# Kernel optimization log

Hardware: AMD Instinct MI355X
Metric: run time of the kernel (lower is better)

The kernel has to match this reference:

```python
import jax, jax.numpy as jnp
import numpy as np

# Forest layout: 6 levels, children of node i at level L are contiguous at level L+1.
LEVEL_SIZES = [4096, 16384, 65536, 131072, 262144, 262144]
OFF = np.concatenate([[0], np.cumsum(LEVEL_SIZES)]).astype(np.int64)
N_NODES = int(OFF[-1])
VOCAB = 50000
D_IN = 128
HID = 128
N_CLASS = 4
W_SCALE = 0.08  # keep gate pre-activations in a sane range


def setup_inputs() -> dict:
    key = jax.random.key(0)
    ks = jax.random.split(key, 24)
    inp = {}
    inp["sen"] = jax.random.randint(ks[0], (N_NODES,), 0, VOCAB, dtype=jnp.int32)
    inp["embedding"] = jax.random.normal(ks[1], (VOCAB, D_IN), jnp.float32)
    names = ["ix", "ih", "fx", "fh", "ox", "oh", "ux", "uh"]
    for j, nm in enumerate(names):
        din = D_IN if nm.endswith("x") else HID
        inp["W_" + nm] = jax.random.normal(ks[2 + j], (din, HID), jnp.float32) * W_SCALE
        inp["b_" + nm] = jnp.zeros((HID,), jnp.float32)
    inp["W_out"] = jax.random.normal(ks[20], (HID, N_CLASS), jnp.float32) * W_SCALE
    inp["b_out"] = jnp.zeros((N_CLASS,), jnp.float32)
    return inp


def _forward(sen, embedding, W_ix, b_ix, W_ih, b_ih, W_fx, b_fx, W_fh, b_fh,
             W_ox, b_ox, W_oh, b_oh, W_ux, b_ux, W_uh, b_uh, W_out, b_out):
    emb = embedding[sen]                               # [N, D_in] gather
    h_all = jnp.zeros((N_NODES, HID), emb.dtype)
    c_all = jnp.zeros((N_NODES, HID), emb.dtype)
    L_last = len(LEVEL_SIZES) - 1
    for L in range(L_last, -1, -1):                    # bottom-up over levels
        o0, o1 = int(OFF[L]), int(OFF[L + 1])
        nL = LEVEL_SIZES[L]
        x = emb[o0:o1]                                 # [nL, D_in]
        if L == L_last:                                # leaves: no children
            h_sum = jnp.zeros((nL, HID), emb.dtype)
            fc_sum = jnp.zeros((nL, HID), emb.dtype)
        else:
            c0, c1 = int(OFF[L + 1]), int(OFF[L + 2])
            ratio = LEVEL_SIZES[L + 1] // nL           # children per node
            hc = h_all[c0:c1].reshape(nL, ratio, HID)  # children h
            cc = c_all[c0:c1].reshape(nL, ratio, HID)  # children c
            h_sum = hc.sum(axis=1)
            # per-child forget gate: sigmoid(fx(x_parent) + fh(h_child))
            f = jax.nn.sigmoid((x @ W_fx + b_fx)[:, None, :] + hc @ W_fh + b_fh)
            fc_sum = (f * cc).sum(axis=1)
        i = jax.nn.sigmoid(x @ W_ix + b_ix + h_sum @ W_ih + b_ih)
        og = jax.nn.sigmoid(x @ W_ox + b_ox + h_sum @ W_oh + b_oh)
        u = jnp.tanh(x @ W_ux + b_ux + h_sum @ W_uh + b_uh)
        c = i * u + fc_sum
        h = og * jnp.tanh(c)
        h_all = h_all.at[o0:o1].set(h)
        c_all = c_all.at[o0:o1].set(c)
    root_h = h_all[: LEVEL_SIZES[0]]                   # level-0 nodes
    return root_h @ W_out + b_out                      # [n_roots, 4] logits


def reference(sen, embedding, W_ix, b_ix, W_ih, b_ih, W_fx, b_fx, W_fh, b_fh,
              W_ox, b_ox, W_oh, b_oh, W_ux, b_ux, W_uh, b_uh, W_out, b_out):
    return _forward(sen, embedding, W_ix, b_ix, W_ih, b_ih, W_fx, b_fx, W_fh, b_fh,
                    W_ox, b_ox, W_oh, b_oh, W_ux, b_ux, W_uh, b_uh, W_out, b_out)
```

## Files before the change

### kernel.cpp

```cpp
#include <hip/hip_runtime.h>
#include <hip/hip_bf16.h>
#include <cstdio>

typedef unsigned short u16;
typedef __bf16 bf16x8 __attribute__((ext_vector_type(8)));
typedef float  floatx4 __attribute__((ext_vector_type(4)));

__device__ __forceinline__ float bf2f(u16 u) {
  union { unsigned int i; float f; } v; v.i = ((unsigned int)u) << 16; return v.f;
}
__device__ __forceinline__ u16 f2bf(float f) {
  union { float f; unsigned int i; } v; v.f = f;
  unsigned int x = v.i;
  return (u16)((x + 0x7fffu + ((x >> 16) & 1u)) >> 16);
}
__device__ __forceinline__ unsigned int f2bf_pk(float a, float b) {
  __hip_bfloat162 h = __float22bfloat162_rn(make_float2(a, b));
  union { __hip_bfloat162 h; unsigned int u; } v; v.h = h; return v.u;
}
__device__ __forceinline__ float sigmoidf_(float x) {
  return __builtin_amdgcn_rcpf(1.f + __expf(-x));
}
__device__ __forceinline__ float tanhf_(float x) {
  return fmaf(-2.f, __builtin_amdgcn_rcpf(1.f + __expf(2.f * x)), 1.f);
}

__device__ __forceinline__ int swz128(int row, int c16) {
  return row * 128 + ((c16 ^ (row & 15)) << 3);
}
__device__ __forceinline__ int swze(int row, int col) {
  return row * 128 + (((((col >> 3)) ^ (row & 15)) << 3) | (col & 7));
}

__global__ __launch_bounds__(256, 2) void proj_e(
    const float* __restrict__ emb, const u16* __restrict__ WT,
    const float* __restrict__ bsum, u16* __restrict__ Ep,
    u16* __restrict__ Hl, u16* __restrict__ Cl)
{
  __shared__ __align__(16) u16 ldsA[128 * 128];
  const int tid = threadIdx.x;
  const long m0 = (long)blockIdx.x * 128;
  {
    const int r = tid >> 1, half = tid & 1;
    long row = m0 + r; if (row > 49999) row = 49999;
    const float* src = emb + row * 128 + half * 64;
#pragma unroll
    for (int i = 0; i < 8; i++) {
      float4 v0 = *reinterpret_cast<const float4*>(src + i * 8);
      float4 v1 = *reinterpret_cast<const float4*>(src + i * 8 + 4);
      unsigned int ov[4] = { f2bf_pk(v0.x, v0.y), f2bf_pk(v0.z, v0.w),
                             f2bf_pk(v1.x, v1.y), f2bf_pk(v1.z, v1.w) };
      *reinterpret_cast<uint4*>(&ldsA[swz128(r, half * 8 + i)]) =
          *reinterpret_cast<const uint4*>(ov);
    }
  }
  __syncthreads();
  const int lane = tid & 63, w = tid >> 6, l16 = lane & 15, quad = lane >> 4;
#pragma unroll
  for (int half = 0; half < 2; half++) {
    const int col = w * 32 + half * 16 + l16;
    bf16x8 bI[4], bU[4], bO[4], bF[4];
#pragma unroll
    for (int ks = 0; ks < 4; ks++) {
      const size_t o_ = ks * 32 + quad * 8;
      bI[ks] = *reinterpret_cast<const bf16x8*>(WT + (size_t)(0   + col) * 128 + o_);
      bU[ks] = *reinterpret_cast<const bf16x8*>(WT + (size_t)(128 + col) * 128 + o_);
      bO[ks] = *reinterpret_cast<const bf16x8*>(WT + (size_t)(256 + col) * 128 + o_);
      bF[ks] = *reinterpret_cast<const bf16x8*>(WT + (size_t)(384 + col) * 128 + o_);
    }
    const float bi = bsum[col], bu = bsum[128 + col], bo = bsum[256 + col], bf = bsum[384 + col];
#pragma unroll
    for (int i = 0; i < 8; i++) {
      floatx4 aI = {0.f,0.f,0.f,0.f}, aU = {0.f,0.f,0.f,0.f};
      floatx4 aO = {0.f,0.f,0.f,0.f}, aF = {0.f,0.f,0.f,0.f};
#pragma unroll
      for (int ks = 0; ks < 4; ks++) {
        bf16x8 a = *reinterpret_cast<const bf16x8*>(&ldsA[swz128(i * 16 + l16, ks * 4 + quad)]);
        aI = __builtin_amdgcn_mfma_f32_16x16x32_bf16(a, bI[ks], aI, 0, 0, 0);
        aU = __builtin_amdgcn_mfma_f32_16x16x32_bf16(a, bU[ks], aU, 0, 0, 0);
        aO = __builtin_amdgcn_mfma_f32_16x16x32_bf16(a, bO[ks], aO, 0, 0, 0);
        aF = __builtin_amdgcn_mfma_f32_16x16x32_bf16(a, bF[ks], aF, 0, 0, 0);
      }
#pragma unroll
      for (int r2 = 0; r2 < 4; r2++) {
        const long row = m0 + i * 16 + quad * 4 + r2;
        if (row < 50000) {
          u16 ov[4] = { f2bf(aI[r2] + bi), f2bf(aU[r2] + bu),
                        f2bf(aO[r2] + bo), f2bf(aF[r2] + bf) };
          *reinterpret_cast<ushort4*>(Ep + row * 512 + col * 4) =
              *reinterpret_cast<const ushort4*>(ov);
          const float cv = sigmoidf_(bf2f(ov[0])) * tanhf_(bf2f(ov[1]));
          const float hv = sigmoidf_(bf2f(ov[2])) * tanhf_(cv);
          Cl[row * 128 + col] = f2bf(cv);
          Hl[row * 128 + col] = f2bf(hv);
        }
      }
    }
  }
}

__global__ __launch_bounds__(256, 2) void k_l3fused(
    const int* __restrict__ sen, const u16* __restrict__ Ep,
    const u16* __restrict__ Hl, const u16* __restrict__ Cl,
    const u16* __restrict__ BfT, const u16* __restrict__ BihT,
    const u16* __restrict__ BuhT, const u16* __restrict__ BohT,
    u16* __restrict__ c_out, u16* __restrict__ h_out,
    long o0, long o1, long o2)
{
  constexpr int PM = 32, CM = 64, NCI = 4, RT = 2;
  __shared__ __align__(16) u16 ldsH[CM * 128];
  __shared__ __align__(16) u16 ldsC[CM * 128];
  __shared__ __align__(16) u16 ldsA[CM * 128];
  __shared__ int sidC[CM];
  __shared__ int sidP[PM];

  const int tid = threadIdx.x;
  const long p0 = (long)blockIdx.x * PM;
  const long cb = (long)blockIdx.x * CM;

  {
    const int r = (tid & 127) >> 1, half = tid & 1;
    const size_t vc = (size_t)sen[o2 + cb + r];
    if (tid < 128) {
      const u16* hs = Hl + vc * 128;
#pragma unroll
      for (int ii = 0; ii < 8; ii++) {
        const int c16 = half * 8 + ii;
        *reinterpret_cast<uint4*>(&ldsH[swz128(r, c16)]) =
            *reinterpret_cast<const uint4*>(hs + c16 * 8);
      }
    } else {
      const u16* cs = Cl + vc * 128;
#pragma unroll
      for (int ii = 0; ii < 8; ii++) {
        const int c16 = half * 8 + ii;
        *reinterpret_cast<uint4*>(&ldsC[swz128(r, c16)]) =
            *reinterpret_cast<const uint4*>(cs + c16 * 8);
      }
    }
    if (tid < CM) sidC[tid] = sen[o1 + cb + tid];
    if (tid < PM) sidP[tid] = sen[o0 + p0 + tid];
  }
  __syncthreads();

  const int lane = tid & 63, w = tid >> 6, l16 = lane & 15, quad = lane >> 4;

#define LDE(I,R2) (*reinterpret_cast<const ushort4*>( \
    Ep + (size_t)sidC[(I) * 16 + quad * 4 + (R2)] * 512 + col * 4))
#define EPI1(R2, E) { \
    const int row = rbase + (R2); \
    const float iv = sigmoidf_(aI[R2] + bf2f((E).x)); \
    const float uv = tanhf_   (aU[R2] + bf2f((E).y)); \
    const float ov = sigmoidf_(aO[R2] + bf2f((E).z)); \
    const float fv = sigmoidf_(aF[R2] + bf2f((E).w)); \
    const int sl = swze(row, col); \
    const float c4 = fmaf(iv, uv, fv * bf2f(ldsC[sl])); \
    const float h4 = ov * tanhf_(c4); \
    ldsC[sl] = f2bf(c4); \
    ldsA[sl] = f2bf(h4); \
  }
#pragma unroll
  for (int gl = 0; gl < 2; gl++) {
    const int col = w * 32 + gl * 16 + l16;
    ushort4 e0 = LDE(0, 0), e1 = LDE(0, 1), e2 = LDE(0, 2), e3 = LDE(0, 3);
    bf16x8 hI[4], hU[4], hO[4], hF[4];
#pragma unroll
    for (int ks = 0; ks < 4; ks++) {
      const size_t ho = (size_t)col * 128 + ks * 32 + quad * 8;
      hI[ks] = *reinterpret_cast<const bf16x8*>(BihT + ho);
      hU[ks] = *reinterpret_cast<const bf16x8*>(BuhT + ho);
      hO[ks] = *reinterpret_cast<const bf16x8*>(BohT + ho);
      hF[ks] = *reinterpret_cast<const bf16x8*>(BfT  + ho);
    }
#pragma unroll
    for (int i = 0; i < NCI; i++) {
      ushort4 n0 = e0, n1 = e1, n2 = e2, n3 = e3;
      if (i + 1 < NCI) {
        n0 = LDE(i + 1, 0); n1 = LDE(i + 1, 1);
        n2 = LDE(i + 1, 2); n3 = LDE(i + 1, 3);
      }
      floatx4 aI = {0.f,0.f,0.f,0.f}, aU = {0.f,0.f,0.f,0.f};
      floatx4 aO = {0.f,0.f,0.f,0.f}, aF = {0.f,0.f,0.f,0.f};
#pragma unroll
      for (int ks = 0; ks < 4; ks++) {
        bf16x8 ah = *reinterpret_cast<const bf16x8*>(&ldsH[swz128(i * 16 + l16, ks * 4 + quad)]);
        aI = __builtin_amdgcn_mfma_f32_16x16x32_bf16(ah, hI[ks], aI, 0, 0, 0);
        aU = __builtin_amdgcn_mfma_f32_16x16x32_bf16(ah, hU[ks], aU, 0, 0, 0);
        aO = __builtin_amdgcn_mfma_f32_16x16x32_bf16(ah, hO[ks], aO, 0, 0, 0);
        aF = __builtin_amdgcn_mfma_f32_16x16x32_bf16(ah, hF[ks], aF, 0, 0, 0);
      }
      const int rbase = i * 16 + quad * 4;
      EPI1(0, e0) EPI1(1, e1) EPI1(2, e2) EPI1(3, e3)
      e0 = n0; e1 = n1; e2 = n2; e3 = n3;
    }
  }
#undef LDE
#undef EPI1
  __syncthreads();

#define LDG(I,T) (*reinterpret_cast<const ushort4*>( \
    Ep + (size_t)sidP[(((I) * 16 + quad * 4) >> 1) + (T)] * 512 + col * 4))
#define EPI2(T, G) { \
    const int p = (rbase >> 1) + (T); \
    const float epf = bf2f((G).w); \
    float fsum = 0.f, isum = 0.f, usum = 0.f, osum = 0.f; \
    _Pragma("unroll") \
    for (int r2 = (T) * RT; r2 < (T) * RT + RT; r2++) { \
      const int row = rbase + r2; \
      const float cch = bf2f(ldsC[swze(row, col)]); \
      fsum += sigmoidf_(aF[r2] + epf) * cch; \
      isum += aI[r2]; usum += aU[r2]; osum += aO[r2]; \
    } \
    const float c = sigmoidf_(isum + bf2f((G).x)) * tanhf_(usum + bf2f((G).y)) + fsum; \
    const float h = sigmoidf_(osum + bf2f((G).z)) * tanhf_(c); \
    c_out[(p0 + p) * 128 + col] = f2bf(c); \
    h_out[(p0 + p) * 128 + col] = f2bf(h); \
  }
#pragma unroll
  for (int gl = 0; gl < 2; gl++) {
    const int col = w * 32 + gl * 16 + l16;
    ushort4 g0 = LDG(0, 0), g1 = LDG(0, 1);
    bf16x8 bF[4], bI[4], bU[4], bO[4];
#pragma unroll
    for (int ks = 0; ks < 4; ks++) {
      const size_t bo_ = (size_t)col * 128 + ks * 32 + quad * 8;
      bF[ks] = *reinterpret_cast<const bf16x8*>(BfT + bo_);
      bI[ks] = *reinterpret_cast<const bf16x8*>(BihT + bo_);
      bU[ks] = *reinterpret_cast<const bf16x8*>(BuhT + bo_);
      bO[ks] = *reinterpret_cast<const bf16x8*>(BohT + bo_);
    }
#pragma unroll
    for (int i = 0; i < NCI; i++) {
      ushort4 m0 = g0, m1 = g1;
      if (i + 1 < NCI) { m0 = LDG(i + 1, 0); m1 = LDG(i + 1, 1); }
      floatx4 aF = {0.f,0.f,0.f,0.f}, aI = {0.f,0.f,0.f,0.f};
      floatx4 aU = {0.f,0.f,0.f,0.f}, aO = {0.f,0.f,0.f,0.f};
#pragma unroll
      for (int ks = 0; ks < 4; ks++) {
        bf16x8 a = *reinterpret_cast<const bf16x8*>(&ldsA[swz128(i * 16 + l16, ks * 4 + quad)]);
        aF = __builtin_amdgcn_mfma_f32_16x16x32_bf16(a, bF[ks], aF, 0, 0, 0);
        aI = __builtin_amdgcn_mfma_f32_16x16x32_bf16(a, bI[ks], aI, 0, 0, 0);
        aU = __builtin_amdgcn_mfma_f32_16x16x32_bf16(a, bU[ks], aU, 0, 0, 0);
        aO = __builtin_amdgcn_mfma_f32_16x16x32_bf16(a, bO[ks], aO, 0, 0, 0);
      }
      const int rbase = i * 16 + quad * 4;
      EPI2(0, g0) EPI2(1, g1)
      g0 = m0; g1 = m1;
    }
  }
#undef LDG
#undef EPI2
}

template<int LR>
__global__ __launch_bounds__(256, 2) void k_level(
    const int* __restrict__ sen, const u16* __restrict__ Ep,
    const u16* __restrict__ h_prev, const u16* __restrict__ c_prev,
    const u16* __restrict__ BfT, const u16* __restrict__ BihT,
    const u16* __restrict__ BuhT, const u16* __restrict__ BohT,
    u16* __restrict__ c_out, u16* __restrict__ h_out,
    long o0)
{
  constexpr int PM  = (LR == 2) ? 32 : 64;
  constexpr int CM  = PM << LR;
  constexpr int NCI = CM / 16;
  constexpr int RT  = 1 << LR;
  constexpr int RTI = 4 >> LR;
  constexpr int TPR = 256 / CM;
  __shared__ __align__(16) u16 ldsA[CM * 128];
  __shared__ int sidP[PM];

  const int tid = threadIdx.x;
  const long p0 = (long)blockIdx.x * PM;
  const long cb = (long)blockIdx.x * CM;

  {
    const int r = tid / TPR, q = tid % TPR;
    constexpr int CH = 16 / TPR;
    const u16* src = h_prev + (cb + r) * 128;
#pragma unroll
    for (int ii = 0; ii < CH; ii++) {
      const int c16 = q * CH + ii;
      *reinterpret_cast<uint4*>(&ldsA[swz128(r, c16)]) =
          *reinterpret_cast<const uint4*>(src + c16 * 8);
    }
    if (tid < PM) sidP[tid] = sen[o0 + p0 + tid];
  }
  __syncthreads();

  const int lane = tid & 63, w = tid >> 6, l16 = lane & 15, quad = lane >> 4;

#pragma unroll
  for (int gl = 0; gl < 2; gl++) {
    const int col = w * 32 + gl * 16 + l16;
    bf16x8 bF[4], bI[4], bU[4], bO[4];
#pragma unroll
    for (int ks = 0; ks < 4; ks++) {
      const size_t bo_ = (size_t)col * 128 + ks * 32 + quad * 8;
      bF[ks] = *reinterpret_cast<const bf16x8*>(BfT + bo_);
      bI[ks] = *reinterpret_cast<const bf16x8*>(BihT + bo_);
      bU[ks] = *reinterpret_cast<const bf16x8*>(BuhT + bo_);
      bO[ks] = *reinterpret_cast<const bf16x8*>(BohT + bo_);
    }
#pragma unroll
    for (int i = 0; i < NCI; i++) {
      const int rbase = i * 16 + quad * 4;
      ushort4 g4p[RTI];
      u16 cch16[RTI][RT];
#pragma unroll
      for (int t = 0; t < RTI; t++) {
        g4p[t] = *reinterpret_cast<const ushort4*>(
            Ep + (size_t)sidP[(rbase >> LR) + t] * 512 + col * 4);
#pragma unroll
        for (int r2 = 0; r2 < RT; r2++)
          cch16[t][r2] = c_prev[(cb + rbase + t * RT + r2) * 128 + col];
      }
      floatx4 aF = {0.f,0.f,0.f,0.f}, aI = {0.f,0.f,0.f,0.f};
      floatx4 aU = {0.f,0.f,0.f,0.f}, aO = {0.f,0.f,0.f,0.f};
#pragma unroll
      for (int ks = 0; ks < 4; ks++) {
        bf16x8 a = *reinterpret_cast<const bf16x8*>(&ldsA[swz128(i * 16 + l16, ks * 4 + quad)]);
        aF = __builtin_amdgcn_mfma_f32_16x16x32_bf16(a, bF[ks], aF, 0, 0, 0);
        aI = __builtin_amdgcn_mfma_f32_16x16x32_bf16(a, bI[ks], aI, 0, 0, 0);
        aU = __builtin_amdgcn_mfma_f32_16x16x32_bf16(a, bU[ks], aU, 0, 0, 0);
        aO = __builtin_amdgcn_mfma_f32_16x16x32_bf16(a, bO[ks], aO, 0, 0, 0);
      }
#pragma unroll
      for (int t = 0; t < RTI; t++) {
        const int p = (rbase >> LR) + t;
        const ushort4 g4 = g4p[t];
        const float epf = bf2f(g4.w);
        float fsum = 0.f, isum = 0.f, usum = 0.f, osum = 0.f;
#pragma unroll
        for (int r2 = t * RT; r2 < t * RT + RT; r2++) {
          const float cch = bf2f(cch16[t][r2 - t * RT]);
          fsum += sigmoidf_(aF[r2] + epf) * cch;
          isum += aI[r2]; usum += aU[r2]; osum += aO[r2];
        }
        const float c = sigmoidf_(isum + bf2f(g4.x)) * tanhf_(usum + bf2f(g4.y)) + fsum;
        const float h = sigmoidf_(osum + bf2f(g4.z)) * tanhf_(c);
        c_out[(p0 + p) * 128 + col] = f2bf(c);
        h_out[(p0 + p) * 128 + col] = f2bf(h);
      }
    }
  }
}

__global__ void build_prep(
    const float* __restrict__ Wix, const float* __restrict__ Wux,
    const float* __restrict__ Wox, const float* __restrict__ Wfx,
    const float* __restrict__ Wih, const float* __restrict__ Wuh,
    const float* __restrict__ Woh, const float* __restrict__ Wfh,
    const float* __restrict__ b_ix, const float* __restrict__ b_ih,
    const float* __restrict__ b_ux, const float* __restrict__ b_uh,
    const float* __restrict__ b_ox, const float* __restrict__ b_oh,
    const float* __restrict__ b_fx, const float* __restrict__ b_fh,
    u16* __restrict__ WT, u16* __restrict__ BihT, u16* __restrict__ BuhT,
    u16* __restrict__ BohT, u16* __restrict__ BfhT, float* __restrict__ bsum)
{
  const int idx = blockIdx.x * 256 + threadIdx.x;
  if (idx < 65536) {
    int n = idx >> 7, k = idx & 127;
    int g = n >> 7, j = n & 127;
    const float* W = (g == 0) ? Wix : (g == 1) ? Wux : (g == 2) ? Wox : Wfx;
    WT[idx] = f2bf(W[k * 128 + j]);
  } else if (idx < 131072) {
    int t = idx - 65536;
    int tb = t >> 14, i2 = t & 16383;
    int n = i2 >> 7, k = i2 & 127;
    const float* W = (tb == 0) ? Wih : (tb == 1) ? Wuh : (tb == 2) ? Woh : Wfh;
    u16* BT = (tb == 0) ? BihT : (tb == 1) ? BuhT : (tb == 2) ? BohT : BfhT;
    BT[i2] = f2bf(W[k * 128 + n]);
  } else if (idx < 131584) {
    int s = idx - 131072;
    int g = s >> 7, j = s & 127;
    float v = (g == 0) ? b_ix[j] + b_ih[j] : (g == 1) ? b_ux[j] + b_uh[j]
            : (g == 2) ? b_ox[j] + b_oh[j] : b_fx[j] + b_fh[j];
    bsum[s] = v;
  }
}

__global__ void out_proj(const u16* __restrict__ h_root, const float* __restrict__ W_out,
                         const float* __restrict__ b_out, float* __restrict__ out)
{
  int idx = blockIdx.x * 256 + threadIdx.x;
  int n = idx >> 2, cls = idx & 3;
  float s = b_out[cls];
  for (int k = 0; k < 128; k++)
    s += bf2f(h_root[(long)n * 128 + k]) * W_out[k * 4 + cls];
  out[idx] = s;
}

extern "C" void kernel_launch(void* const* d_in, const int* in_sizes, int n_in,
                              void* d_out, int out_size, void* d_ws, size_t ws_size,
                              hipStream_t stream)
{
  const int*   sen  = (const int*)d_in[0];
  const float* emb  = (const float*)d_in[1];
  const float* W_ix = (const float*)d_in[2];  const float* b_ix = (const float*)d_in[3];
  const float* W_ih = (const float*)d_in[4];  const float* b_ih = (const float*)d_in[5];
  const float* W_fx = (const float*)d_in[6];  const float* b_fx = (const float*)d_in[7];
  const float* W_fh = (const float*)d_in[8];  const float* b_fh = (const float*)d_in[9];
  const float* W_ox = (const float*)d_in[10]; const float* b_ox = (const float*)d_in[11];
  const float* W_oh = (const float*)d_in[12]; const float* b_oh = (const float*)d_in[13];
  const float* W_ux = (const float*)d_in[14]; const float* b_ux = (const float*)d_in[15];
  const float* W_uh = (const float*)d_in[16]; const float* b_uh = (const float*)d_in[17];
  const float* W_out= (const float*)d_in[18]; const float* b_out= (const float*)d_in[19];
  float* out = (float*)d_out;

  const size_t EPB = (size_t)50000 * 512 * 2;
  const size_t TBB = (size_t)50000 * 128 * 2;
  const size_t H3  = (size_t)131072 * 128 * 2;
  const size_t H2  = (size_t)65536  * 128 * 2;
  const size_t H1  = (size_t)16384  * 128 * 2;
  const size_t H0  = (size_t)4096   * 128 * 2;
  const size_t need = EPB + 2 * TBB + 2 * (H3 + H2 + H1 + H0)
                    + (size_t)512 * 128 * 2 + 4 * (size_t)128 * 128 * 2 + 512 * 4 + 8192;
  fprintf(stderr, "[tree_lstm] ws_size=%zu need=%zu\n", ws_size, need);
  if (ws_size < need) {
    fprintf(stderr, "[tree_lstm] INSUFFICIENT WORKSPACE — skipping launch\n");
    return;
  }
  char* ws = (char*)d_ws;
  size_t off = 0;
  auto take = [&](size_t bytes) { char* p = ws + off; off += (bytes + 255) & ~(size_t)255; return p; };
  u16* Ep = (u16*)take(EPB);
  u16* Hl = (u16*)take(TBB);
  u16* Cl = (u16*)take(TBB);
  u16* h3 = (u16*)take(H3);  u16* c3 = (u16*)take(H3);
  u16* h2 = (u16*)take(H2);  u16* c2 = (u16*)take(H2);
  u16* h1 = (u16*)take(H1);  u16* c1 = (u16*)take(H1);
  u16* h0 = (u16*)take(H0);  u16* c0 = (u16*)take(H0);
  u16* WallT = (u16*)take((size_t)512 * 128 * 2);
  u16* BihT = (u16*)take((size_t)128 * 128 * 2);
  u16* BuhT = (u16*)take((size_t)128 * 128 * 2);
  u16* BohT = (u16*)take((size_t)128 * 128 * 2);
  u16* BfhT = (u16*)take((size_t)128 * 128 * 2);
  float* bsum = (float*)take(512 * 4);

  build_prep<<<514, 256, 0, stream>>>(W_ix, W_ux, W_ox, W_fx, W_ih, W_uh, W_oh, W_fh,
      b_ix, b_ih, b_ux, b_uh, b_ox, b_oh, b_fx, b_fh,
      WallT, BihT, BuhT, BohT, BfhT, bsum);
  proj_e<<<391, 256, 0, stream>>>(emb, WallT, bsum, Ep, Hl, Cl);

  const long LOFF[6] = {0, 4096, 20480, 86016, 217088, 479232};

  k_l3fused<<<4096, 256, 0, stream>>>(sen, Ep, Hl, Cl,
      BfhT, BihT, BuhT, BohT, c3, h3, LOFF[3], LOFF[4], LOFF[5]);
  k_level<1><<<1024, 256, 0, stream>>>(sen, Ep, h3, c3,
      BfhT, BihT, BuhT, BohT, c2, h2, LOFF[2]);
  k_level<2><<<512, 256, 0, stream>>>(sen, Ep, h2, c2,
      BfhT, BihT, BuhT, BohT, c1, h1, LOFF[1]);
  k_level<2><<<128, 256, 0, stream>>>(sen, Ep, h1, c1,
      BfhT, BihT, BuhT, BohT, c0, h0, LOFF[0]);

  out_proj<<<64, 256, 0, stream>>>(h0, W_out, b_out, out);
}
```

Before: 476.4 us.

## Fuse all tree levels into one per-root kernel keeping h/c in LDS

Replaces the level-3 fused kernel and three per-level kernels with a single kernel where each block owns one root's whole subtree (64 leaves down to 1 root). Intermediate h and c stay in LDS ping-pong buffers instead of being written to and re-read from global memory, and three kernel launches disappear. In exchange the upper levels run tiny MFMA tiles with many idle lanes (root level uses only one quad) and more syncthreads per block. The per-level global workspace is removed.

```diff
diff --git a/kernel.cpp b/kernel.cpp
--- a/kernel.cpp
+++ b/kernel.cpp
@@ -99,34 +99,32 @@
   }
 }
 
-__global__ __launch_bounds__(256, 2) void k_l3fused(
+__global__ __launch_bounds__(256, 2) void k_tree(
     const int* __restrict__ sen, const u16* __restrict__ Ep,
     const u16* __restrict__ Hl, const u16* __restrict__ Cl,
     const u16* __restrict__ BfT, const u16* __restrict__ BihT,
     const u16* __restrict__ BuhT, const u16* __restrict__ BohT,
-    u16* __restrict__ c_out, u16* __restrict__ h_out,
-    long o0, long o1, long o2)
+    u16* __restrict__ h_root,
+    long o0, long o1, long o2, long o3, long o4, long o5)
 {
-  constexpr int PM = 32, CM = 64, NCI = 4, RT = 2;
-  __shared__ __align__(16) u16 ldsH[CM * 128];
-  __shared__ __align__(16) u16 ldsC[CM * 128];
-  __shared__ __align__(16) u16 ldsA[CM * 128];
-  __shared__ int sidC[CM];
-  __shared__ int sidP[PM];
+  __shared__ __align__(16) u16 bufH0[64 * 128];
+  __shared__ __align__(16) u16 bufH1[64 * 128];
+  __shared__ __align__(16) u16 cbuf [64 * 128];
+  __shared__ int sidL4[64], sidL3[32], sidL2[16], sidL1[4], sidL0v[1];
 
   const int tid = threadIdx.x;
-  const long p0 = (long)blockIdx.x * PM;
-  const long cb = (long)blockIdx.x * CM;
+  const long b  = blockIdx.x;
+  const long cb = b * 64;
 
   {
     const int r = (tid & 127) >> 1, half = tid & 1;
-    const size_t vc = (size_t)sen[o2 + cb + r];
+    const size_t vc = (size_t)sen[o5 + cb + r];
     if (tid < 128) {
       const u16* hs = Hl + vc * 128;
 #pragma unroll
       for (int ii = 0; ii < 8; ii++) {
         const int c16 = half * 8 + ii;
-        *reinterpret_cast<uint4*>(&ldsH[swz128(r, c16)]) =
+        *reinterpret_cast<uint4*>(&bufH0[swz128(r, c16)]) =
             *reinterpret_cast<const uint4*>(hs + c16 * 8);
       }
     } else {
@@ -134,19 +132,22 @@
 #pragma unroll
       for (int ii = 0; ii < 8; ii++) {
         const int c16 = half * 8 + ii;
-        *reinterpret_cast<uint4*>(&ldsC[swz128(r, c16)]) =
+        *reinterpret_cast<uint4*>(&cbuf[swz128(r, c16)]) =
             *reinterpret_cast<const uint4*>(cs + c16 * 8);
       }
     }
-    if (tid < CM) sidC[tid] = sen[o1 + cb + tid];
-    if (tid < PM) sidP[tid] = sen[o0 + p0 + tid];
+    if (tid < 64)        sidL4[tid]       = sen[o4 + cb + tid];
+    else if (tid < 96)   sidL3[tid - 64]  = sen[o3 + b * 32 + (tid - 64)];
+    else if (tid < 112)  sidL2[tid - 96]  = sen[o2 + b * 16 + (tid - 96)];
+    else if (tid < 116)  sidL1[tid - 112] = sen[o1 + b * 4 + (tid - 112)];
+    else if (tid == 116) sidL0v[0]        = sen[o0 + b];
   }
   __syncthreads();
 
   const int lane = tid & 63, w = tid >> 6, l16 = lane & 15, quad = lane >> 4;
 
 #define LDE(I,R2) (*reinterpret_cast<const ushort4*>( \
-    Ep + (size_t)sidC[(I) * 16 + quad * 4 + (R2)] * 512 + col * 4))
+    Ep + (size_t)sidL4[(I) * 16 + quad * 4 + (R2)] * 512 + col * 4))
 #define EPI1(R2, E) { \
     const int row = rbase + (R2); \
     const float iv = sigmoidf_(aI[R2] + bf2f((E).x)); \
@@ -154,10 +155,10 @@
     const float ov = sigmoidf_(aO[R2] + bf2f((E).z)); \
     const float fv = sigmoidf_(aF[R2] + bf2f((E).w)); \
     const int sl = swze(row, col); \
-    const float c4 = fmaf(iv, uv, fv * bf2f(ldsC[sl])); \
+    const float c4 = fmaf(iv, uv, fv * bf2f(cbuf[sl])); \
     const float h4 = ov * tanhf_(c4); \
-    ldsC[sl] = f2bf(c4); \
-    ldsA[sl] = f2bf(h4); \
+    cbuf[sl] = f2bf(c4); \
+    bufH1[sl] = f2bf(h4); \
   }
 #pragma unroll
   for (int gl = 0; gl < 2; gl++) {
@@ -173,9 +174,9 @@
       hF[ks] = *reinterpret_cast<const bf16x8*>(BfT  + ho);
     }
 #pragma unroll
-    for (int i = 0; i < NCI; i++) {
+    for (int i = 0; i < 4; i++) {
       ushort4 n0 = e0, n1 = e1, n2 = e2, n3 = e3;
-      if (i + 1 < NCI) {
+      if (i + 1 < 4) {
         n0 = LDE(i + 1, 0); n1 = LDE(i + 1, 1);
         n2 = LDE(i + 1, 2); n3 = LDE(i + 1, 3);
       }
@@ -183,7 +184,7 @@
       floatx4 aO = {0.f,0.f,0.f,0.f}, aF = {0.f,0.f,0.f,0.f};
 #pragma unroll
       for (int ks = 0; ks < 4; ks++) {
-        bf16x8 ah = *reinterpret_cast<const bf16x8*>(&ldsH[swz128(i * 16 + l16, ks * 4 + quad)]);
+        bf16x8 ah = *reinterpret_cast<const bf16x8*>(&bufH0[swz128(i * 16 + l16, ks * 4 + quad)]);
         aI = __builtin_amdgcn_mfma_f32_16x16x32_bf16(ah, hI[ks], aI, 0, 0, 0);
         aU = __builtin_amdgcn_mfma_f32_16x16x32_bf16(ah, hU[ks], aU, 0, 0, 0);
         aO = __builtin_amdgcn_mfma_f32_16x16x32_bf16(ah, hO[ks], aO, 0, 0, 0);
@@ -198,149 +199,218 @@
 #undef EPI1
   __syncthreads();
 
+  {
+    float tc2[16];
 #define LDG(I,T) (*reinterpret_cast<const ushort4*>( \
-    Ep + (size_t)sidP[(((I) * 16 + quad * 4) >> 1) + (T)] * 512 + col * 4))
-#define EPI2(T, G) { \
+    Ep + (size_t)sidL3[(((I) * 16 + quad * 4) >> 1) + (T)] * 512 + col * 4))
+#define EPI2(I, T, G) { \
+    const int rbase = (I) * 16 + quad * 4; \
     const int p = (rbase >> 1) + (T); \
     const float epf = bf2f((G).w); \
     float fsum = 0.f, isum = 0.f, usum = 0.f, osum = 0.f; \
     _Pragma("unroll") \
-    for (int r2 = (T) * RT; r2 < (T) * RT + RT; r2++) { \
-      const int row = rbase + r2; \
-      const float cch = bf2f(ldsC[swze(row, col)]); \
+    for (int r2 = (T) * 2; r2 < (T) * 2 + 2; r2++) { \
+      const float cch = bf2f(cbuf[swze(rbase + r2, col)]); \
       fsum += sigmoidf_(aF[r2] + epf) * cch; \
       isum += aI[r2]; usum += aU[r2]; osum += aO[r2]; \
     } \
     const float c = sigmoidf_(isum + bf2f((G).x)) * tanhf_(usum + bf2f((G).y)) + fsum; \
     const float h = sigmoidf_(osum + bf2f((G).z)) * tanhf_(c); \
-    c_out[(p0 + p) * 128 + col] = f2bf(c); \
-    h_out[(p0 + p) * 128 + col] = f2bf(h); \
-  }
-#pragma unroll
-  for (int gl = 0; gl < 2; gl++) {
-    const int col = w * 32 + gl * 16 + l16;
-    ushort4 g0 = LDG(0, 0), g1 = LDG(0, 1);
-    bf16x8 bF[4], bI[4], bU[4], bO[4];
-#pragma unroll
-    for (int ks = 0; ks < 4; ks++) {
-      const size_t bo_ = (size_t)col * 128 + ks * 32 + quad * 8;
-      bF[ks] = *reinterpret_cast<const bf16x8*>(BfT + bo_);
-      bI[ks] = *reinterpret_cast<const bf16x8*>(BihT + bo_);
-      bU[ks] = *reinterpret_cast<const bf16x8*>(BuhT + bo_);
-      bO[ks] = *reinterpret_cast<const bf16x8*>(BohT + bo_);
-    }
-#pragma unroll
-    for (int i = 0; i < NCI; i++) {
-      ushort4 m0 = g0, m1 = g1;
-      if (i + 1 < NCI) { m0 = LDG(i + 1, 0); m1 = LDG(i + 1, 1); }
+    bufH0[swze(p, col)] = f2bf(h); \
+    tc2[(I) * 2 + (T) + gl * 8] = c; \
+  }
+#pragma unroll
+    for (int gl = 0; gl < 2; gl++) {
+      const int col = w * 32 + gl * 16 + l16;
+      ushort4 g0 = LDG(0, 0), g1 = LDG(0, 1);
+      bf16x8 bF[4], bI[4], bU[4], bO[4];
+#pragma unroll
+      for (int ks = 0; ks < 4; ks++) {
+        const size_t bo_ = (size_t)col * 128 + ks * 32 + quad * 8;
+        bF[ks] = *reinterpret_cast<const bf16x8*>(BfT + bo_);
+        bI[ks] = *reinterpret_cast<const bf16x8*>(BihT + bo_);
+        bU[ks] = *reinterpret_cast<const bf16x8*>(BuhT + bo_);
+        bO[ks] = *reinterpret_cast<const bf16x8*>(BohT + bo_);
+      }
+#pragma unroll
+      for (int i = 0; i < 4; i++) {
+        ushort4 m0 = g0, m1 = g1;
+        if (i + 1 < 4) { m0 = LDG(i + 1, 0); m1 = LDG(i + 1, 1); }
+        floatx4 aF = {0.f,0.f,0.f,0.f}, aI = {0.f,0.f,0.f,0.f};
+        floatx4 aU = {0.f,0.f,0.f,0.f}, aO = {0.f,0.f,0.f,0.f};
+#pragma unroll
+        for (int ks = 0; ks < 4; ks++) {
+          bf16x8 a = *reinterpret_cast<const bf16x8*>(&bufH1[swz128(i * 16 + l16, ks * 4 + quad)]);
+          aF = __builtin_amdgcn_mfma_f32_16x16x32_bf16(a, bF[ks], aF, 0, 0, 0);
+          aI = __builtin_amdgcn_mfma_f32_16x16x32_bf16(a, bI[ks], aI, 0, 0, 0);
+          aU = __builtin_amdgcn_mfma_f32_16x16x32_bf16(a, bU[ks], aU, 0, 0, 0);
+          aO = __builtin_amdgcn_mfma_f32_16x16x32_bf16(a, bO[ks], aO, 0, 0, 0);
+        }
+        EPI2(i, 0, g0) EPI2(i, 1, g1)
+        g0 = m0; g1 = m1;
+      }
+    }
+#undef LDG
+#undef EPI2
+    __syncthreads();
+#pragma unroll
+    for (int gl = 0; gl < 2; gl++) {
+      const int col = w * 32 + gl * 16 + l16;
+#pragma unroll
+      for (int i = 0; i < 4; i++)
+#pragma unroll
+        for (int t = 0; t < 2; t++)
+          cbuf[swze(i * 8 + quad * 2 + t, col)] = f2bf(tc2[i * 2 + t + gl * 8]);
+    }
+    __syncthreads();
+  }
+
+  {
+    float tc3[8];
+#pragma unroll
+    for (int gl = 0; gl < 2; gl++) {
+      const int col = w * 32 + gl * 16 + l16;
+      bf16x8 bF[4], bI[4], bU[4], bO[4];
+#pragma unroll
+      for (int ks = 0; ks < 4; ks++) {
+        const size_t bo_ = (size_t)col * 128 + ks * 32 + quad * 8;
+        bF[ks] = *reinterpret_cast<const bf16x8*>(BfT + bo_);
+        bI[ks] = *reinterpret_cast<const bf16x8*>(BihT + bo_);
+        bU[ks] = *reinterpret_cast<const bf16x8*>(BuhT + bo_);
+        bO[ks] = *reinterpret_cast<const bf16x8*>(BohT + bo_);
+      }
+#pragma unroll
+      for (int i = 0; i < 2; i++) {
+        floatx4 aF = {0.f,0.f,0.f,0.f}, aI = {0.f,0.f,0.f,0.f};
+        floatx4 aU = {0.f,0.f,0.f,0.f}, aO = {0.f,0.f,0.f,0.f};
+#pragma unroll
+        for (int ks = 0; ks < 4; ks++) {
+          bf16x8 a = *reinterpret_cast<const bf16x8*>(&bufH0[swz128(i * 16 + l16, ks * 4 + quad)]);
+          aF = __builtin_amdgcn_mfma_f32_16x16x32_bf16(a, bF[ks], aF, 0, 0, 0);
+          aI = __builtin_amdgcn_mfma_f32_16x16x32_bf16(a, bI[ks], aI, 0, 0, 0);
+          aU = __builtin_amdgcn_mfma_f32_16x16x32_bf16(a, bU[ks], aU, 0, 0, 0);
+          aO = __builtin_amdgcn_mfma_f32_16x16x32_bf16(a, bO[ks], aO, 0, 0, 0);
+        }
+        const int rbase = i * 16 + quad * 4;
+#pragma unroll
+        for (int t = 0; t < 2; t++) {
+          const int p = (rbase >> 1) + t;
+          ushort4 g4 = *reinterpret_cast<const ushort4*>(
+              Ep + (size_t)sidL2[p] * 512 + col * 4);
+          const float epf = bf2f(g4.w);
+          float fsum = 0.f, isum = 0.f, usum = 0.f, osum = 0.f;
+#pragma unroll
+          for (int r2 = t * 2; r2 < t * 2 + 2; r2++) {
+            const float cch = bf2f(cbuf[swze(rbase + r2, col)]);
+            fsum += sigmoidf_(aF[r2] + epf) * cch;
+            isum += aI[r2]; usum += aU[r2]; osum += aO[r2];
+          }
+          const float c = sigmoidf_(isum + bf2f(g4.x)) * tanhf_(usum + bf2f(g4.y)) + fsum;
+          const float h = sigmoidf_(osum + bf2f(g4.z)) * tanhf_(c);
+          bufH1[swze(p, col)] = f2bf(h);
+          tc3[gl * 4 + i * 2 + t] = c;
+        }
+      }
+    }
+    __syncthreads();
+#pragma unroll
+    for (int gl = 0; gl < 2; gl++) {
+      const int col = w * 32 + gl * 16 + l16;
+#pragma unroll
+      for (int i = 0; i < 2; i++)
+#pragma unroll
+        for (int t = 0; t < 2; t++)
+          cbuf[swze(i * 8 + quad * 2 + t, col)] = f2bf(tc3[gl * 4 + i * 2 + t]);
+    }
+    __syncthreads();
+  }
+
+  {
+    float tc4[2];
+#pragma unroll
+    for (int gl = 0; gl < 2; gl++) {
+      const int col = w * 32 + gl * 16 + l16;
+      bf16x8 bF[4], bI[4], bU[4], bO[4];
+#pragma unroll
+      for (int ks = 0; ks < 4; ks++) {
+        const size_t bo_ = (size_t)col * 128 + ks * 32 + quad * 8;
+        bF[ks] = *reinterpret_cast<const bf16x8*>(BfT + bo_);
+        bI[ks] = *reinterpret_cast<const bf16x8*>(BihT + bo_);
+        bU[ks] = *reinterpret_cast<const bf16x8*>(BuhT + bo_);
+        bO[ks] = *reinterpret_cast<const bf16x8*>(BohT + bo_);
+      }
       floatx4 aF = {0.f,0.f,0.f,0.f}, aI = {0.f,0.f,0.f,0.f};
       floatx4 aU = {0.f,0.f,0.f,0.f}, aO = {0.f,0.f,0.f,0.f};
 #pragma unroll
       for (int ks = 0; ks < 4; ks++) {
-        bf16x8 a = *reinterpret_cast<const bf16x8*>(&ldsA[swz128(i * 16 + l16, ks * 4 + quad)]);
+        bf16x8 a = *reinterpret_cast<const bf16x8*>(&bufH1[swz128(l16, ks * 4 + quad)]);
         aF = __builtin_amdgcn_mfma_f32_16x16x32_bf16(a, bF[ks], aF, 0, 0, 0);
         aI = __builtin_amdgcn_mfma_f32_16x16x32_bf16(a, bI[ks], aI, 0, 0, 0);
         aU = __builtin_amdgcn_mfma_f32_16x16x32_bf16(a, bU[ks], aU, 0, 0, 0);
         aO = __builtin_amdgcn_mfma_f32_16x16x32_bf16(a, bO[ks], aO, 0, 0, 0);
       }
-      const int rbase = i * 16 + quad * 4;
-      EPI2(0, g0) EPI2(1, g1)
-      g0 = m0; g1 = m1;
-    }
-  }
-#undef LDG
-#undef EPI2
-}
-
-template<int LR>
-__global__ __launch_bounds__(256, 2) void k_level(
-    const int* __restrict__ sen, const u16* __restrict__ Ep,
-    const u16* __restrict__ h_prev, const u16* __restrict__ c_prev,
-    const u16* __restrict__ BfT, const u16* __restrict__ BihT,
-    const u16* __restrict__ BuhT, const u16* __restrict__ BohT,
-    u16* __restrict__ c_out, u16* __restrict__ h_out,
-    long o0)
-{
-  constexpr int PM  = (LR == 2) ? 32 : 64;
-  constexpr int CM  = PM << LR;
-  constexpr int NCI = CM / 16;
-  constexpr int RT  = 1 << LR;
-  constexpr int RTI = 4 >> LR;
-  constexpr int TPR = 256 / CM;
-  __shared__ __align__(16) u16 ldsA[CM * 128];
-  __shared__ int sidP[PM];
-
-  const int tid = threadIdx.x;
-  const long p0 = (long)blockIdx.x * PM;
-  const long cb = (long)blockIdx.x * CM;
+      const int rbase = quad * 4, p = quad;
+      ushort4 g4 = *reinterpret_cast<const ushort4*>(
+          Ep + (size_t)sidL1[p] * 512 + col * 4);
+      const float epf = bf2f(g4.w);
+      float fsum = 0.f, isum = 0.f, usum = 0.f, osum = 0.f;
+#pragma unroll
+      for (int r2 = 0; r2 < 4; r2++) {
+        const float cch = bf2f(cbuf[swze(rbase + r2, col)]);
+        fsum += sigmoidf_(aF[r2] + epf) * cch;
+        isum += aI[r2]; usum += aU[r2]; osum += aO[r2];
+      }
+      const float c = sigmoidf_(isum + bf2f(g4.x)) * tanhf_(usum + bf2f(g4.y)) + fsum;
+      const float h = sigmoidf_(osum + bf2f(g4.z)) * tanhf_(c);
+      bufH0[swze(p, col)] = f2bf(h);
+      tc4[gl] = c;
+    }
+    __syncthreads();
+#pragma unroll
+    for (int gl = 0; gl < 2; gl++) {
+      const int col = w * 32 + gl * 16 + l16;
+      cbuf[swze(quad, col)] = f2bf(tc4[gl]);
+    }
+    __syncthreads();
+  }
 
   {
-    const int r = tid / TPR, q = tid % TPR;
-    constexpr int CH = 16 / TPR;
-    const u16* src = h_prev + (cb + r) * 128;
-#pragma unroll
-    for (int ii = 0; ii < CH; ii++) {
-      const int c16 = q * CH + ii;
-      *reinterpret_cast<uint4*>(&ldsA[swz128(r, c16)]) =
-          *reinterpret_cast<const uint4*>(src + c16 * 8);
-    }
-    if (tid < PM) sidP[tid] = sen[o0 + p0 + tid];
-  }
-  __syncthreads();
-
-  const int lane = tid & 63, w = tid >> 6, l16 = lane & 15, quad = lane >> 4;
-
-#pragma unroll
-  for (int gl = 0; gl < 2; gl++) {
-    const int col = w * 32 + gl * 16 + l16;
-    bf16x8 bF[4], bI[4], bU[4], bO[4];
-#pragma unroll
-    for (int ks = 0; ks < 4; ks++) {
-      const size_t bo_ = (size_t)col * 128 + ks * 32 + quad * 8;
-      bF[ks] = *reinterpret_cast<const bf16x8*>(BfT + bo_);
-      bI[ks] = *reinterpret_cast<const bf16x8*>(BihT + bo_);
-      bU[ks] = *reinterpret_cast<const bf16x8*>(BuhT + bo_);
-      bO[ks] = *reinterpret_cast<const bf16x8*>(BohT + bo_);
-    }
-#pragma unroll
-    for (int i = 0; i < NCI; i++) {
-      const int rbase = i * 16 + quad * 4;
-      ushort4 g4p[RTI];
-      u16 cch16[RTI][RT];
-#pragma unroll
-      for (int t = 0; t < RTI; t++) {
-        g4p[t] = *reinterpret_cast<const ushort4*>(
-            Ep + (size_t)sidP[(rbase >> LR) + t] * 512 + col * 4);
-#pragma unroll
-        for (int r2 = 0; r2 < RT; r2++)
-          cch16[t][r2] = c_prev[(cb + rbase + t * RT + r2) * 128 + col];
+#pragma unroll
+    for (int gl = 0; gl < 2; gl++) {
+      const int col = w * 32 + gl * 16 + l16;
+      bf16x8 bF[4], bI[4], bU[4], bO[4];
+#pragma unroll
+      for (int ks = 0; ks < 4; ks++) {
+        const size_t bo_ = (size_t)col * 128 + ks * 32 + quad * 8;
+        bF[ks] = *reinterpret_cast<const bf16x8*>(BfT + bo_);
+        bI[ks] = *reinterpret_cast<const bf16x8*>(BihT + bo_);
+        bU[ks] = *reinterpret_cast<const bf16x8*>(BuhT + bo_);
+        bO[ks] = *reinterpret_cast<const bf16x8*>(BohT + bo_);
       }
       floatx4 aF = {0.f,0.f,0.f,0.f}, aI = {0.f,0.f,0.f,0.f};
       floatx4 aU = {0.f,0.f,0.f,0.f}, aO = {0.f,0.f,0.f,0.f};
 #pragma unroll
       for (int ks = 0; ks < 4; ks++) {
-        bf16x8 a = *reinterpret_cast<const bf16x8*>(&ldsA[swz128(i * 16 + l16, ks * 4 + quad)]);
+        bf16x8 a = *reinterpret_cast<const bf16x8*>(&bufH0[swz128(l16, ks * 4 + quad)]);
         aF = __builtin_amdgcn_mfma_f32_16x16x32_bf16(a, bF[ks], aF, 0, 0, 0);
         aI = __builtin_amdgcn_mfma_f32_16x16x32_bf16(a, bI[ks], aI, 0, 0, 0);
         aU = __builtin_amdgcn_mfma_f32_16x16x32_bf16(a, bU[ks], aU, 0, 0, 0);
         aO = __builtin_amdgcn_mfma_f32_16x16x32_bf16(a, bO[ks], aO, 0, 0, 0);
       }
-#pragma unroll
-      for (int t = 0; t < RTI; t++) {
-        const int p = (rbase >> LR) + t;
-        const ushort4 g4 = g4p[t];
+      if (quad == 0) {
+        ushort4 g4 = *reinterpret_cast<const ushort4*>(
+            Ep + (size_t)sidL0v[0] * 512 + col * 4);
         const float epf = bf2f(g4.w);
         float fsum = 0.f, isum = 0.f, usum = 0.f, osum = 0.f;
 #pragma unroll
-        for (int r2 = t * RT; r2 < t * RT + RT; r2++) {
-          const float cch = bf2f(cch16[t][r2 - t * RT]);
+        for (int r2 = 0; r2 < 4; r2++) {
+          const float cch = bf2f(cbuf[swze(r2, col)]);
           fsum += sigmoidf_(aF[r2] + epf) * cch;
           isum += aI[r2]; usum += aU[r2]; osum += aO[r2];
         }
         const float c = sigmoidf_(isum + bf2f(g4.x)) * tanhf_(usum + bf2f(g4.y)) + fsum;
         const float h = sigmoidf_(osum + bf2f(g4.z)) * tanhf_(c);
-        c_out[(p0 + p) * 128 + col] = f2bf(c);
-        h_out[(p0 + p) * 128 + col] = f2bf(h);
+        h_root[b * 128 + col] = f2bf(h);
       }
     }
   }
@@ -410,11 +480,8 @@
 
   const size_t EPB = (size_t)50000 * 512 * 2;
   const size_t TBB = (size_t)50000 * 128 * 2;
-  const size_t H3  = (size_t)131072 * 128 * 2;
-  const size_t H2  = (size_t)65536  * 128 * 2;
-  const size_t H1  = (size_t)16384  * 128 * 2;
-  const size_t H0  = (size_t)4096   * 128 * 2;
-  const size_t need = EPB + 2 * TBB + 2 * (H3 + H2 + H1 + H0)
+  const size_t HRB = (size_t)4096 * 128 * 2;
+  const size_t need = EPB + 2 * TBB + HRB
                     + (size_t)512 * 128 * 2 + 4 * (size_t)128 * 128 * 2 + 512 * 4 + 8192;
   fprintf(stderr, "[tree_lstm] ws_size=%zu need=%zu\n", ws_size, need);
   if (ws_size < need) {
@@ -427,10 +494,7 @@
   u16* Ep = (u16*)take(EPB);
   u16* Hl = (u16*)take(TBB);
   u16* Cl = (u16*)take(TBB);
-  u16* h3 = (u16*)take(H3);  u16* c3 = (u16*)take(H3);
-  u16* h2 = (u16*)take(H2);  u16* c2 = (u16*)take(H2);
-  u16* h1 = (u16*)take(H1);  u16* c1 = (u16*)take(H1);
-  u16* h0 = (u16*)take(H0);  u16* c0 = (u16*)take(H0);
+  u16* hroot = (u16*)take(HRB);
   u16* WallT = (u16*)take((size_t)512 * 128 * 2);
   u16* BihT = (u16*)take((size_t)128 * 128 * 2);
   u16* BuhT = (u16*)take((size_t)128 * 128 * 2);
@@ -445,14 +509,9 @@
 
   const long LOFF[6] = {0, 4096, 20480, 86016, 217088, 479232};
 
-  k_l3fused<<<4096, 256, 0, stream>>>(sen, Ep, Hl, Cl,
-      BfhT, BihT, BuhT, BohT, c3, h3, LOFF[3], LOFF[4], LOFF[5]);
-  k_level<1><<<1024, 256, 0, stream>>>(sen, Ep, h3, c3,
-      BfhT, BihT, BuhT, BohT, c2, h2, LOFF[2]);
-  k_level<2><<<512, 256, 0, stream>>>(sen, Ep, h2, c2,
-      BfhT, BihT, BuhT, BohT, c1, h1, LOFF[1]);
-  k_level<2><<<128, 256, 0, stream>>>(sen, Ep, h1, c1,
-      BfhT, BihT, BuhT, BohT, c0, h0, LOFF[0]);
-
-  out_proj<<<64, 256, 0, stream>>>(h0, W_out, b_out, out);
-}
+  k_tree<<<4096, 256, 0, stream>>>(sen, Ep, Hl, Cl,
+      BfhT, BihT, BuhT, BohT, hroot,
+      LOFF[0], LOFF[1], LOFF[2], LOFF[3], LOFF[4], LOFF[5]);
+
+  out_proj<<<64, 256, 0, stream>>>(hroot, W_out, b_out, out);
+}
```

Measured after the change: 579.0 us. 21.5% more time.
